# Performance work log

Hardware: AMD Instinct MI355X
Metric: run time of the kernel (lower is better)

Reference implementation:

```python
import jax, jax.numpy as jnp
import numpy as np

D_MODEL = 512; D_STATE = 128; D_CONV = 4; EXPAND = 2; HEADDIM = 64; CHUNK = 64
D_INNER = EXPAND * D_MODEL            # 1024
NHEADS = D_INNER // HEADDIM           # 16
CONV_DIM = D_INNER + 2 * D_STATE      # 1280
D_IN_PROJ = 2 * D_INNER + 2 * D_STATE + NHEADS  # 2320
BATCH, SEQLEN = 2, 8192


def setup_inputs() -> dict:
    key = jax.random.key(0)
    ks = jax.random.split(key, 8)
    s = 0.02
    return {
        "x": jax.random.normal(ks[0], (BATCH, SEQLEN, D_MODEL), jnp.float32),
        "in_proj_w": jax.random.normal(ks[1], (D_IN_PROJ, D_MODEL), jnp.float32) * s,
        "conv_w": jax.random.normal(ks[2], (CONV_DIM, 1, D_CONV), jnp.float32) * s,
        "conv_b": jnp.zeros((CONV_DIM,), jnp.float32),
        "dt_bias": jax.random.normal(ks[3], (NHEADS,), jnp.float32) * s,
        "A_log": jnp.log(jnp.arange(1, NHEADS + 1, dtype=jnp.float32)),
        "D_skip": jnp.ones((NHEADS,), jnp.float32),
        "norm_w": jnp.ones((D_INNER,), jnp.float32),
        "ssm_out_w": jax.random.normal(ks[4], (D_MODEL, D_INNER), jnp.float32) * s,
        "fuse_w": jax.random.normal(ks[5], (D_MODEL, 2 * D_MODEL), jnp.float32) * s,
        "fuse_b": jnp.zeros((D_MODEL,), jnp.float32),
    }


def segsum(a):
    # a: (..., T) -> (..., T, T) with [i, j] = sum_{j < d <= i} a[d]; -inf above diag
    T = a.shape[-1]
    a = jnp.broadcast_to(a[..., :, None], a.shape + (T,))
    a = jnp.where(jnp.tril(jnp.ones((T, T), bool), -1), a, 0.0)
    a = jnp.cumsum(a, axis=-2)
    return jnp.where(jnp.tril(jnp.ones((T, T), bool), 0), a, -jnp.inf)


def ssd(x, A, B, C):
    # x: (b,l,h,p), A: (b,l,h), B/C: (b,l,n) (single group, broadcast over heads)
    b, l, h, p = x.shape
    c = l // CHUNK
    x = x.reshape(b, c, CHUNK, h, p)
    A = jnp.transpose(A.reshape(b, c, CHUNK, h), (0, 3, 1, 2))   # (b,h,c,s)
    B = B.reshape(b, c, CHUNK, -1)
    C = C.reshape(b, c, CHUNK, -1)
    A_cumsum = jnp.cumsum(A, axis=-1)                             # (b,h,c,s)
    L = jnp.exp(segsum(A))                                        # (b,h,c,s,s) intra-chunk decay
    Y_diag = jnp.einsum("bcln,bcsn,bhcls,bcshp->bclhp", C, B, L, x)
    decay_states = jnp.exp(A_cumsum[..., -1:] - A_cumsum)         # (b,h,c,s)
    states = jnp.einsum("bcln,bhcl,bclhp->bchpn", B, decay_states, x)
    init = jnp.zeros_like(states[:, :1])
    A_pad = jnp.pad(A_cumsum[..., -1], ((0, 0), (0, 0), (1, 0)))  # (b,h,c+1)
    decay_chunk = jnp.exp(segsum(A_pad))                          # (b,h,c+1,c+1)
    new_states = jnp.einsum("bhzc,bchpn->bzhpn", decay_chunk,
                            jnp.concatenate([init, states], axis=1))
    states = new_states[:, :-1]                                   # state entering each chunk
    state_decay_out = jnp.exp(A_cumsum)
    Y_off = jnp.einsum("bchpn,bcsn,bhcs->bcshp", states, C, state_decay_out)
    return (Y_diag + Y_off).reshape(b, l, h, p)


def mamba2_block(u, in_proj_w, conv_w, conv_b, dt_bias, A_log, D_skip, norm_w, ssm_out_w):
    b, l, _ = u.shape
    zxbcdt = u @ in_proj_w.T                                      # (b,l,2320)
    z = zxbcdt[..., :D_INNER]
    xBC = zxbcdt[..., D_INNER:D_INNER + CONV_DIM]
    dt = jax.nn.softplus(zxbcdt[..., -NHEADS:] + dt_bias)         # (b,l,h)
    # depthwise causal conv over time
    conv = jax.lax.conv_general_dilated(
        jnp.transpose(xBC, (0, 2, 1)), conv_w, (1,), [(D_CONV - 1, 0)],
        dimension_numbers=("NCH", "OIH", "NCH"), feature_group_count=CONV_DIM)
    xBC = jax.nn.silu(jnp.transpose(conv + conv_b[None, :, None], (0, 2, 1)))
    xh = xBC[..., :D_INNER].reshape(b, l, NHEADS, HEADDIM)
    Bm = xBC[..., D_INNER:D_INNER + D_STATE]
    Cm = xBC[..., -D_STATE:]
    A = -jnp.exp(A_log)                                           # (h,)
    y = ssd(xh * dt[..., None], A * dt, Bm, Cm)
    y = y + xh * D_skip[None, None, :, None]
    y = y.reshape(b, l, D_INNER)
    # gated RMSNorm
    y = y * jax.nn.silu(z)
    y = y * jax.lax.rsqrt(jnp.mean(y * y, axis=-1, keepdims=True) + 1e-5) * norm_w
    return y @ ssm_out_w.T


def reference(x, in_proj_w, conv_w, conv_b, dt_bias, A_log, D_skip, norm_w,
              ssm_out_w, fuse_w, fuse_b):
    args = (in_proj_w, conv_w, conv_b, dt_bias, A_log, D_skip, norm_w, ssm_out_w)
    y_fwd = mamba2_block(x, *args)
    y_rev = jnp.flip(mamba2_block(jnp.flip(x, 1), *args), 1)
    y_cat = jnp.concatenate([y_fwd, y_rev], axis=-1)
    return y_cat @ fuse_w.T + fuse_b
```

## Files before the change

kernel.cpp:

```cpp
#include <hip/hip_runtime.h>
#include <cstddef>

#define B_SZ     2
#define L_SEQ    8192
#define D_INNERC 1024
#define D_CAT    2048
#define NHEADSC  16
#define CHUNKC   64
#define NCHUNKC  128
#define CONV_DIMC 1280
#define D_PROJC  2320
#define M_ROWS   16384

typedef unsigned short bfu;

using bf16x8 = __attribute__((ext_vector_type(8))) short;
using f32x4  = __attribute__((ext_vector_type(4))) float;

__device__ __forceinline__ float silu_(float v) { return v / (1.f + expf(-v)); }

__device__ __forceinline__ float b2f(bfu u) {
  return __uint_as_float((unsigned)u << 16);
}
__device__ __forceinline__ bfu f2b(float f) {
  unsigned x = __float_as_uint(f);
  return (bfu)((x + 0x7fffu + ((x >> 16) & 1u)) >> 16);
}

__device__ __forceinline__ float4 ld4(const float* p) { return *(const float4*)p; }
__device__ __forceinline__ float4 ld4(const bfu* p) {
  ushort4 u = *(const ushort4*)p;
  float4 f;
  f.x = b2f(u.x); f.y = b2f(u.y); f.z = b2f(u.z); f.w = b2f(u.w);
  return f;
}
__device__ __forceinline__ void st4(float* p, float4 v) { *(float4*)p = v; }
__device__ __forceinline__ void st4(bfu* p, float4 v) {
  ushort4 u;
  u.x = f2b(v.x); u.y = f2b(v.y); u.z = f2b(v.z); u.w = f2b(v.w);
  *(ushort4*)p = u;
}

__device__ __forceinline__ void gl_lds16(const bfu* g, bfu* l) {
  __builtin_amdgcn_global_load_lds(
      (const __attribute__((address_space(1))) unsigned int*)g,
      (__attribute__((address_space(3))) unsigned int*)l, 16, 0, 0);
}

__device__ __forceinline__ int pos_of(int b, int c, int l, int dir) {
  int t = c * CHUNKC + l;
  return dir ? (b * L_SEQ + (L_SEQ - 1) - t) : (b * L_SEQ + t);
}

__global__ __launch_bounds__(256)
void mfma_nt(const bfu* __restrict__ A, int lda,
             const bfu* __restrict__ Bw, int ldb,
             void* __restrict__ Cv, int ldc,
             int N, int K, const float* __restrict__ bias, int mode)
{
  __shared__ bfu sh[16384];
  bfu* As = sh;
  bfu* Bs = sh + 8192;
  const int tid  = threadIdx.x;
  const int lane = tid & 63;
  const int wave = __builtin_amdgcn_readfirstlane(tid >> 6);
  const int wm = wave & 1, wn = wave >> 1;

  const int num_n = gridDim.x;
  const int flat  = blockIdx.y * num_n + blockIdx.x;
  const int xcd   = flat & 7;
  const int g     = flat >> 3;
  const int n0 = (g % num_n) * 128;
  const int m0 = ((g / num_n) * 8 + xcd) * 128;

  f32x4 acc[4][4];
#pragma unroll
  for (int i = 0; i < 4; ++i)
#pragma unroll
    for (int j = 0; j < 4; ++j)
      acc[i][j] = (f32x4){0.f, 0.f, 0.f, 0.f};

  const int ro   = lane >> 3;
  const int slot = lane & 7;

  for (int k0 = 0; k0 < K; k0 += 64) {
    __syncthreads();
#pragma unroll
    for (int si = 0; si < 4; ++si) {
      int r = wave * 32 + si * 8 + ro;
      int cg = slot ^ (r & 7);
      gl_lds16(A  + (size_t)(m0 + r) * lda + k0 + cg * 8, As + (wave * 32 + si * 8) * 64);
      gl_lds16(Bw + (size_t)(n0 + r) * ldb + k0 + cg * 8, Bs + (wave * 32 + si * 8) * 64);
    }
    __syncthreads();

#pragma unroll
    for (int ks = 0; ks < 2; ++ks) {
      bf16x8 af[4], bfr[4];
#pragma unroll
      for (int i = 0; i < 4; ++i) {
        int ra = wm * 64 + i * 16 + (lane & 15);
        int ca = (ks * 4 + (lane >> 4)) ^ (ra & 7);
        af[i] = *(const bf16x8*)(As + ra * 64 + ca * 8);
        int rb = wn * 64 + i * 16 + (lane & 15);
        int cb = (ks * 4 + (lane >> 4)) ^ (rb & 7);
        bfr[i] = *(const bf16x8*)(Bs + rb * 64 + cb * 8);
      }
#pragma unroll
      for (int i = 0; i < 4; ++i)
#pragma unroll
        for (int j = 0; j < 4; ++j)
          acc[i][j] = __builtin_amdgcn_mfma_f32_16x16x32_bf16(af[i], bfr[j], acc[i][j], 0, 0, 0);
    }
  }

  __syncthreads();
  if (mode == 0) {
#pragma unroll
    for (int i = 0; i < 4; ++i)
#pragma unroll
      for (int j = 0; j < 4; ++j)
#pragma unroll
        for (int r = 0; r < 4; ++r) {
          int ml = wm * 64 + i * 16 + (lane >> 4) * 4 + r;
          int nl = wn * 64 + j * 16 + (lane & 15);
          sh[ml * 128 + nl] = f2b(acc[i][j][r]);
        }
    __syncthreads();
    bfu* Cb = (bfu*)Cv;
#pragma unroll
    for (int rr = 0; rr < 8; ++rr) {
      int idx = rr * 256 + tid;
      int row = idx >> 4, co = (idx & 15) * 8;
      if (n0 + co < N) {
        *(ulonglong2*)(Cb + (size_t)(m0 + row) * ldc + n0 + co) =
            *(const ulonglong2*)(sh + row * 128 + co);
      }
    }
  } else {
    float* Cf = (float*)Cv;
    float* shf = (float*)sh;
#pragma unroll
    for (int p = 0; p < 2; ++p) {
      if (wm == p) {
#pragma unroll
        for (int i = 0; i < 4; ++i)
#pragma unroll
          for (int j = 0; j < 4; ++j)
#pragma unroll
            for (int r = 0; r < 4; ++r) {
              int ml = i * 16 + (lane >> 4) * 4 + r;
              int nl = wn * 64 + j * 16 + (lane & 15);
              shf[ml * 128 + nl] = acc[i][j][r];
            }
      }
      __syncthreads();
#pragma unroll
      for (int rr = 0; rr < 8; ++rr) {
        int idx = rr * 256 + tid;
        int row = idx >> 5, co = (idx & 31) * 4;
        int n = n0 + co;
        if (n < N) {
          float4 v = *(float4*)(shf + row * 128 + co);
          float* cp = Cf + (size_t)(m0 + p * 64 + row) * ldc + n;
          if (bias) {
            v.x += bias[n]; v.y += bias[n + 1]; v.z += bias[n + 2]; v.w += bias[n + 3];
          }
          *(float4*)cp = v;
        }
      }
      __syncthreads();
    }
  }
}

__global__ __launch_bounds__(512)
void mfma_nt_8p(const bfu* __restrict__ A, int lda,
                const bfu* __restrict__ Bw, int ldb,
                bfu* __restrict__ C, int ldc, int N, int K)
{
  __shared__ bfu sh[65536];
  bfu* As0 = sh;
  bfu* As1 = sh + 16384;
  bfu* Bs0 = sh + 32768;
  bfu* Bs1 = sh + 49152;

  const int tid  = threadIdx.x;
  const int lane = tid & 63;
  const int w    = __builtin_amdgcn_readfirstlane(tid >> 6);
  const int wm = w & 1, wn = w >> 1;
  const int q = lane >> 4, t = lane & 15;

  const int num_n = gridDim.x;
  const int flat  = blockIdx.y * num_n + blockIdx.x;
  const int xcd   = flat & 7;
  const int g     = flat >> 3;
  const int n0 = (g % num_n) * 256;
  const int m0 = ((g / num_n) * 8 + xcd) * 256;

  auto STG = [&](const bfu* __restrict__ X, int ldx, int x0, int kt, int h,
                 bfu* dst) {
#pragma unroll
    for (int ci = 0; ci < 2; ++ci) {
      int rb = h * 128 + ci * 64 + w * 8;
      int r  = rb + (lane >> 3);
      int cg = (lane & 7) ^ (r & 7);
      gl_lds16(X + (size_t)(x0 + r) * ldx + kt * 64 + cg * 8, dst + rb * 64);
    }
  };
  auto FR = [&](const bfu* tile, int R, int gg) -> bf16x8 {
    return *(const bf16x8*)(tile + R * 64 + ((gg ^ (R & 7)) * 8));
  };

  f32x4 acc[8][4];
#pragma unroll
  for (int i = 0; i < 8; ++i)
#pragma unroll
    for (int j = 0; j < 4; ++j)
      acc[i][j] = (f32x4){0.f, 0.f, 0.f, 0.f};

  STG(Bw, ldb, n0, 0, 0, Bs0); STG(Bw, ldb, n0, 0, 1, Bs0);
  STG(A,  lda, m0, 0, 0, As0); STG(A,  lda, m0, 0, 1, As0);
  STG(Bw, ldb, n0, 1, 0, Bs1); STG(Bw, ldb, n0, 1, 1, Bs1);
  asm volatile("s_waitcnt vmcnt(4)" ::: "memory");
  __builtin_amdgcn_s_barrier();

  const int nIter = K >> 7;
  bf16x8 bfr[4][2];
  for (int it = 0; it < nIter; ++it) {
    const int kt = it * 2;
    const bool last = (it == nIter - 1);

#pragma unroll
    for (int p = 0; p < 4; ++p) {
      bf16x8 af[2][2];
#pragma unroll
      for (int ii = 0; ii < 2; ++ii)
#pragma unroll
        for (int ks = 0; ks < 2; ++ks)
          af[ii][ks] = FR(As0, wm * 128 + (2 * p + ii) * 16 + t, ks * 4 + q);
      if (p == 0) {
#pragma unroll
        for (int j = 0; j < 4; ++j)
#pragma unroll
          for (int ks = 0; ks < 2; ++ks)
            bfr[j][ks] = FR(Bs0, wn * 64 + j * 16 + t, ks * 4 + q);
      }
      if (p == 0)          STG(A,  lda, m0, kt + 1, 0, As1);
      if (p == 1)          STG(A,  lda, m0, kt + 1, 1, As1);
      if (p == 2 && !last) STG(Bw, ldb, n0, kt + 2, 0, Bs0);
      if (p == 3 && !last) STG(Bw, ldb, n0, kt + 2, 1, Bs0);
      if (p == 3) {
        if (last) asm volatile("s_waitcnt vmcnt(0)" ::: "memory");
        else      asm volatile("s_waitcnt vmcnt(4)" ::: "memory");
      }
      __builtin_amdgcn_s_barrier();
      __builtin_amdgcn_s_setprio(1);
#pragma unroll
      for (int ks = 0; ks < 2; ++ks)
#pragma unroll
        for (int ii = 0; ii < 2; ++ii)
#pragma unroll
          for (int j = 0; j < 4; ++j)
            acc[2 * p + ii][j] = __builtin_amdgcn_mfma_f32_16x16x32_bf16(
                af[ii][ks], bfr[j][ks], acc[2 * p + ii][j], 0, 0, 0);
      __builtin_amdgcn_s_setprio(0);
      __builtin_amdgcn_s_barrier();
    }

#pragma unroll
    for (int p = 0; p < 4; ++p) {
      bf16x8 af[2][2];
#pragma unroll
      for (int ii = 0; ii < 2; ++ii)
#pragma unroll
        for (int ks = 0; ks < 2; ++ks)
          af[ii][ks] = FR(As1, wm * 128 + (2 * p + ii) * 16 + t, ks * 4 + q);
      if (p == 0) {
#pragma unroll
        for (int j = 0; j < 4; ++j)
#pragma unroll
          for (int ks = 0; ks < 2; ++ks)
            bfr[j][ks] = FR(Bs1, wn * 64 + j * 16 + t, ks * 4 + q);
      }
      if (p == 0 && !last) STG(A,  lda, m0, kt + 2, 0, As0);
      if (p == 1 && !last) STG(A,  lda, m0, kt + 2, 1, As0);
      if (p == 2 && !last) STG(Bw, ldb, n0, kt + 3, 0, Bs1);
      if (p == 3 && !last) STG(Bw, ldb, n0, kt + 3, 1, Bs1);
      if (p == 3 && !last) asm volatile("s_waitcnt vmcnt(4)" ::: "memory");
      __builtin_amdgcn_s_barrier();
      __builtin_amdgcn_s_setprio(1);
#pragma unroll
      for (int ks = 0; ks < 2; ++ks)
#pragma unroll
        for (int ii = 0; ii < 2; ++ii)
#pragma unroll
          for (int j = 0; j < 4; ++j)
            acc[2 * p + ii][j] = __builtin_amdgcn_mfma_f32_16x16x32_bf16(
                af[ii][ks], bfr[j][ks], acc[2 * p + ii][j], 0, 0, 0);
      __builtin_amdgcn_s_setprio(0);
      __builtin_amdgcn_s_barrier();
    }
  }

#pragma unroll
  for (int i = 0; i < 8; ++i)
#pragma unroll
    for (int j = 0; j < 4; ++j)
#pragma unroll
      for (int r = 0; r < 4; ++r) {
        int ml = wm * 128 + i * 16 + q * 4 + r;
        int nl = wn * 64 + j * 16 + t;
        sh[ml * 256 + nl] = f2b(acc[i][j][r]);
      }
  __syncthreads();
#pragma unroll
  for (int rr = 0; rr < 16; ++rr) {
    int idx = rr * 512 + tid;
    int row = idx >> 5, co = (idx & 31) * 8;
    if (n0 + co < N) {
      *(ulonglong2*)(C + (size_t)(m0 + row) * ldc + n0 + co) =
          *(const ulonglong2*)(sh + row * 256 + co);
    }
  }
}

__global__ __launch_bounds__(256)
void cvt_x_k(const float* __restrict__ in, bfu* __restrict__ out)
{
  int q = blockIdx.x * 256 + threadIdx.x;
  st4(out + (size_t)q * 4, ld4(in + (size_t)q * 4));
}

__global__ __launch_bounds__(256)
void cvt_w_k(const float* __restrict__ in, bfu* __restrict__ out)
{
  int q = blockIdx.x * 256 + threadIdx.x;
  int row = q >> 7, c4 = (q & 127) << 2;
  float4 v = {0.f, 0.f, 0.f, 0.f};
  if (row < D_PROJC) v = ld4(in + (size_t)row * 512 + c4);
  st4(out + (size_t)row * 512 + c4, v);
}

__global__ __launch_bounds__(256)
void transpose_k(const float* __restrict__ in, bfu* __restrict__ out)
{
  int idx = blockIdx.x * 256 + threadIdx.x;
  int j = idx >> 9, k = idx & 511;
  out[idx] = f2b(in[k * 1024 + j]);
}

__global__ __launch_bounds__(256)
void cvt_fuse_k(const float* __restrict__ in, bfu* __restrict__ out)
{
  int q = blockIdx.x * 256 + threadIdx.x;
  int m = q >> 7, kg = (q & 127) << 2;
  int o = m >> 1, dir = m & 1;
  float4 v = ld4(in + (size_t)o * 1024 + dir * 512 + kg);
  st4(out + (size_t)m * 512 + kg, v);
}

__global__ __launch_bounds__(256)
void conv_k(const bfu* __restrict__ zx, const float* __restrict__ conv_w,
            const float* __restrict__ conv_b, bfu* __restrict__ xBC, int dir)
{
  int ch = blockIdx.x * 256 + threadIdx.x;
  int m0 = blockIdx.y * 8;
  int b  = m0 >> 13, tb = m0 & (L_SEQ - 1);
  float w0 = conv_w[ch * 4 + 0], w1 = conv_w[ch * 4 + 1];
  float w2 = conv_w[ch * 4 + 2], w3 = conv_w[ch * 4 + 3];
  float cb = conv_b[ch];
  const bfu* src = zx + 1024 + ch;
  const int shift = dir ? 0 : 3;

  float v[11];
#pragma unroll
  for (int i = 0; i < 11; ++i) {
    int tt = tb + i - shift;
    v[i] = (tt >= 0 && tt < L_SEQ)
         ? b2f(src[(size_t)(b * L_SEQ + tt) * D_PROJC]) : 0.f;
  }
#pragma unroll
  for (int j = 0; j < 8; ++j) {
    float acc = cb;
    if (dir == 0) {
      acc += w0 * v[j] + w1 * v[j + 1] + w2 * v[j + 2] + w3 * v[j + 3];
    } else {
      acc += w0 * v[j + 3] + w1 * v[j + 2] + w2 * v[j + 1] + w3 * v[j];
    }
    xBC[(size_t)(m0 + j) * CONV_DIMC + ch] = f2b(silu_(acc));
  }
}

__global__ __launch_bounds__(256)
void states_mfma_k(const bfu* __restrict__ zx, const bfu* __restrict__ xBC,
                   const float* __restrict__ dt_bias, const float* __restrict__ A_log,
                   float* __restrict__ acum_g, float* __restrict__ dt_g,
                   bfu* __restrict__ states, int dir)
{
  __shared__ bfu BT[128 * 72];
  __shared__ bfu xsT[64 * 72];
  __shared__ float scaleS[8 * 64];

  int bid = blockIdx.x;
  int hb = bid >> 8;
  int c = bid & 127, b = (bid >> 7) & 1;
  int tid = threadIdx.x, lane = tid & 63;
  int w = tid >> 6, q = lane >> 4, t = lane & 15;

#pragma unroll
  for (int rr = 0; rr < 2; ++rr) {
    int i = w + rr * 4;
    int h = hb * 8 + i;
    int l = lane;
    int pos = pos_of(b, c, l, dir);
    float dtr = b2f(zx[(size_t)pos * D_PROJC + 2304 + h]) + dt_bias[h];
    float dt = (dtr > 20.f) ? dtr : log1pf(expf(dtr));
    float a = -expf(A_log[h]) * dt;
#pragma unroll
    for (int off = 1; off < 64; off <<= 1) {
      float v = __shfl_up(a, off);
      if (l >= off) a += v;
    }
    float alast = __shfl(a, 63);
    int gi = ((b * NCHUNKC + c) * NHEADSC + h) * 64 + l;
    acum_g[gi] = a; dt_g[gi] = dt;
    scaleS[i * 64 + l] = dt * expf(alast - a);
  }

#pragma unroll
  for (int r = 0; r < 8; ++r) {
    int qq = tid + r * 256;
    int l = qq & 63, ng = qq >> 6;
    ushort4 v = *(const ushort4*)(xBC + (size_t)pos_of(b, c, l, dir) * CONV_DIMC + 1024 + ng * 4);
    BT[(ng * 4 + 0) * 72 + l] = v.x; BT[(ng * 4 + 1) * 72 + l] = v.y;
    BT[(ng * 4 + 2) * 72 + l] = v.z; BT[(ng * 4 + 3) * 72 + l] = v.w;
  }

  ushort4 xr[4];
  auto PREFX = [&](int i) {
    int h = hb * 8 + i;
#pragma unroll
    for (int r = 0; r < 4; ++r) {
      int qq = tid + r * 256;
      int l = qq & 63, pg = qq >> 6;
      xr[r] = *(const ushort4*)(xBC + (size_t)pos_of(b, c, l, dir) * CONV_DIMC + h * 64 + pg * 4);
    }
  };
  PREFX(0);
  __syncthreads();

  for (int i = 0; i < 8; ++i) {
    int h = hb * 8 + i;
#pragma unroll
    for (int r = 0; r < 4; ++r) {
      int qq = tid + r * 256;
      int l = qq & 63, pg = qq >> 6;
      float s = scaleS[i * 64 + l];
      ushort4 v = xr[r];
      xsT[(pg * 4 + 0) * 72 + l] = f2b(b2f(v.x) * s);
      xsT[(pg * 4 + 1) * 72 + l] = f2b(b2f(v.y) * s);
      xsT[(pg * 4 + 2) * 72 + l] = f2b(b2f(v.z) * s);
      xsT[(pg * 4 + 3) * 72 + l] = f2b(b2f(v.w) * s);
    }
    if (i < 7) PREFX(i + 1);
    __syncthreads();

    bf16x8 axs[2];
#pragma unroll
    for (int ks = 0; ks < 2; ++ks)
      axs[ks] = *(const bf16x8*)(xsT + (w * 16 + t) * 72 + ks * 32 + q * 8);

    f32x4 acc[8];
#pragma unroll
    for (int j = 0; j < 8; ++j) acc[j] = (f32x4){0.f, 0.f, 0.f, 0.f};
#pragma unroll
    for (int ks = 0; ks < 2; ++ks)
#pragma unroll
      for (int j = 0; j < 8; ++j) {
        bf16x8 bB = *(const bf16x8*)(BT + (j * 16 + t) * 72 + ks * 32 + q * 8);
        acc[j] = __builtin_amdgcn_mfma_f32_16x16x32_bf16(axs[ks], bB, acc[j], 0, 0, 0);
      }

    size_t base = ((size_t)(b * NCHUNKC + c) * NHEADSC + h) * 8192;
#pragma unroll
    for (int j = 0; j < 8; ++j)
#pragma unroll
      for (int r = 0; r < 4; ++r) {
        int p = w * 16 + q * 4 + r, n = j * 16 + t;
        states[base + p * 128 + n] = f2b(acc[j][r]);
      }
    __syncthreads();
  }
}

__global__ __launch_bounds__(256)
void scan_k(bfu* __restrict__ states, const float* __restrict__ acum_g)
{
  int bid = blockIdx.x;
  int eb = bid & 15, h = (bid >> 4) & 15, b = bid >> 8;
  int e = eb * 512 + threadIdx.x * 2;
  bfu* p0 = states + ((size_t)(b * NCHUNKC) * NHEADSC + h) * 8192 + e;
  const float* ac = acum_g + ((b * NCHUNKC) * NHEADSC + h) * 64 + 63;
  const size_t cstride = (size_t)NHEADSC * 8192;
  const int astride = NHEADSC * 64;

  float pre0 = 0.f, pre1 = 0.f;
  uint raw = *(const uint*)p0;
  float dcur = expf(ac[0]);
  for (int c = 0; c < NCHUNKC; ++c) {
    uint raw_next = 0; float dnext = 0.f;
    if (c < NCHUNKC - 1) {
      raw_next = *(const uint*)(p0 + (c + 1) * cstride);
      dnext = expf(ac[(c + 1) * astride]);
    }
    float v0 = b2f((bfu)(raw & 0xffff));
    float v1 = b2f((bfu)(raw >> 16));
    uint packed = (uint)f2b(pre0) | ((uint)f2b(pre1) << 16);
    *(uint*)(p0 + c * cstride) = packed;
    pre0 = v0 + dcur * pre0;
    pre1 = v1 + dcur * pre1;
    raw = raw_next; dcur = dnext;
  }
}

__global__ __launch_bounds__(256)
void y_mfma_k(const bfu* __restrict__ xBC, const bfu* __restrict__ states,
              const float* __restrict__ acum_g, const float* __restrict__ dt_g,
              const float* __restrict__ D_skip, bfu* __restrict__ ycat, int dir)
{
  __shared__ bfu smem[30976];
  bfu* Cs  = smem;
  bfu* Bsc = smem + 8704;
  bfu* Ps  = smem + 17408;
  bfu* xhT = smem + 26112;
  float* acumH = (float*)(smem + 30720);
  float* dtH   = acumH + 64;

  int bid = blockIdx.x;
  int hb = bid >> 8;
  int c = bid & 127, b = (bid >> 7) & 1;
  int tid = threadIdx.x, lane = tid & 63;
  int w = tid >> 6, q = lane >> 4, t = lane & 15;

#pragma unroll
  for (int r = 0; r < 8; ++r) {
    int qq = tid + r * 256;
    int row = qq >> 5, grp = qq & 31;
    const bfu* src = xBC + (size_t)pos_of(b, c, row, dir) * CONV_DIMC;
    *(ushort4*)(Cs  + row * 136 + grp * 4) = *(const ushort4*)(src + 1152 + grp * 4);
    *(ushort4*)(Bsc + row * 136 + grp * 4) = *(const ushort4*)(src + 1024 + grp * 4);
  }
  __syncthreads();

  bf16x8 af[4];
#pragma unroll
  for (int ks = 0; ks < 4; ++ks)
    af[ks] = *(const bf16x8*)(Cs + (w * 16 + t) * 136 + ks * 32 + q * 8);

  f32x4 sacc[4];
#pragma unroll
  for (int j = 0; j < 4; ++j) sacc[j] = (f32x4){0.f, 0.f, 0.f, 0.f};
#pragma unroll
  for (int ks = 0; ks < 4; ++ks)
#pragma unroll
    for (int j = 0; j < 4; ++j) {
      bf16x8 bf = *(const bf16x8*)(Bsc + (j * 16 + t) * 136 + ks * 32 + q * 8);
      sacc[j] = __builtin_amdgcn_mfma_f32_16x16x32_bf16(af[ks], bf, sacc[j], 0, 0, 0);
    }

  for (int i = 0; i < 8; ++i) {
    int h = hb * 8 + i;
    __syncthreads();
    size_t pbase = ((size_t)(b * NCHUNKC + c) * NHEADSC + h) * 8192;
#pragma unroll
    for (int r = 0; r < 8; ++r) {
      int qq = tid + r * 256;
      int row = qq >> 5, grp = qq & 31;
      *(ushort4*)(Ps + row * 136 + grp * 4) =
          *(const ushort4*)(states + pbase + row * 128 + grp * 4);
    }
#pragma unroll
    for (int r = 0; r < 4; ++r) {
      int qq = tid + r * 256;
      int l = qq & 63, pg = qq >> 6;
      ushort4 v = *(const ushort4*)(xBC + (size_t)pos_of(b, c, l, dir) * CONV_DIMC + h * 64 + pg * 4);
      xhT[(pg * 4 + 0) * 72 + l] = v.x; xhT[(pg * 4 + 1) * 72 + l] = v.y;
      xhT[(pg * 4 + 2) * 72 + l] = v.z; xhT[(pg * 4 + 3) * 72 + l] = v.w;
    }
    if (tid < 64) {
      int gi = ((b * NCHUNKC + c) * NHEADSC + h) * 64 + tid;
      acumH[tid] = acum_g[gi]; dtH[tid] = dt_g[gi];
    }
    __syncthreads();

    f32x4 yacc[4];
#pragma unroll
    for (int j = 0; j < 4; ++j) yacc[j] = (f32x4){0.f, 0.f, 0.f, 0.f};
#pragma unroll
    for (int ks = 0; ks < 4; ++ks)
#pragma unroll
      for (int j = 0; j < 4; ++j) {
        bf16x8 bP = *(const bf16x8*)(Ps + (j * 16 + t) * 136 + ks * 32 + q * 8);
        yacc[j] = __builtin_amdgcn_mfma_f32_16x16x32_bf16(af[ks], bP, yacc[j], 0, 0, 0);
      }

    float Dh = D_skip[h];
    bfu* sc = Bsc;
#pragma unroll
    for (int j = 0; j < 4; ++j)
#pragma unroll
      for (int r = 0; r < 4; ++r) {
        int l = w * 16 + q * 4 + r, s = j * 16 + t;
        float v = 0.f;
        if (s <= l) v = sacc[j][r] * expf(acumH[l] - acumH[s]) * dtH[s];
        if (s == l) v += Dh;
        sc[l * 72 + s] = f2b(v);
      }

    f32x4 acc2[4];
    float dec[4];
#pragma unroll
    for (int r = 0; r < 4; ++r) dec[r] = expf(acumH[w * 16 + q * 4 + r]);
#pragma unroll
    for (int j = 0; j < 4; ++j)
#pragma unroll
      for (int r = 0; r < 4; ++r) acc2[j][r] = yacc[j][r] * dec[r];

#pragma unroll
    for (int ks = 0; ks < 2; ++ks) {
      bf16x8 asc = *(const bf16x8*)(sc + (w * 16 + t) * 72 + ks * 32 + q * 8);
#pragma unroll
      for (int j = 0; j < 4; ++j) {
        bf16x8 bx = *(const bf16x8*)(xhT + (j * 16 + t) * 72 + ks * 32 + q * 8);
        acc2[j] = __builtin_amdgcn_mfma_f32_16x16x32_bf16(asc, bx, acc2[j], 0, 0, 0);
      }
    }

#pragma unroll
    for (int j = 0; j < 4; ++j)
#pragma unroll
      for (int r = 0; r < 4; ++r) {
        int l = w * 16 + q * 4 + r, p = j * 16 + t;
        ycat[(size_t)pos_of(b, c, l, dir) * D_CAT + dir * 1024 + h * 64 + p] =
            f2b(acc2[j][r]);
      }
  }
}

__global__ __launch_bounds__(256)
void norm_k(bfu* __restrict__ ycat, const bfu* __restrict__ zx,
            const float* __restrict__ norm_w, int dir)
{
  int m = blockIdx.x, tid = threadIdx.x;
  bfu* yp = ycat + (size_t)m * D_CAT + dir * 1024 + tid * 4;
  float4 y = ld4(yp);
  float4 z = ld4(zx + (size_t)m * D_PROJC + tid * 4);
  float4 g;
  g.x = y.x * silu_(z.x); g.y = y.y * silu_(z.y);
  g.z = y.z * silu_(z.z); g.w = y.w * silu_(z.w);
  float ss = g.x * g.x + g.y * g.y + g.z * g.z + g.w * g.w;
#pragma unroll
  for (int off = 32; off >= 1; off >>= 1) ss += __shfl_xor(ss, off);
  __shared__ float red[4];
  int wid = tid >> 6;
  if ((tid & 63) == 0) red[wid] = ss;
  __syncthreads();
  float tot = red[0] + red[1] + red[2] + red[3];
  float scale = rsqrtf(tot * (1.f / 1024.f) + 1e-5f);
  float4 w = *(const float4*)(norm_w + tid * 4);
  g.x *= scale * w.x; g.y *= scale * w.y; g.z *= scale * w.z; g.w *= scale * w.w;
  st4(yp, g);
}

extern "C" void kernel_launch(void* const* d_in, const int* in_sizes, int n_in,
                              void* d_out, int out_size, void* d_ws, size_t ws_size,
                              hipStream_t stream)
{
  const float* x         = (const float*)d_in[0];
  const float* in_proj_w = (const float*)d_in[1];
  const float* conv_w    = (const float*)d_in[2];
  const float* conv_b    = (const float*)d_in[3];
  const float* dt_bias   = (const float*)d_in[4];
  const float* A_log     = (const float*)d_in[5];
  const float* D_skip    = (const float*)d_in[6];
  const float* norm_w    = (const float*)d_in[7];
  const float* ssm_out_w = (const float*)d_in[8];
  const float* fuse_w    = (const float*)d_in[9];
  const float* fuse_b    = (const float*)d_in[10];
  float* out = (float*)d_out;

  bfu* zx     = (bfu*)d_ws;
  bfu* xBC    = zx     + (size_t)M_ROWS * D_PROJC;
  bfu* states = xBC    + (size_t)M_ROWS * CONV_DIMC;
  bfu* ycat   = states + (size_t)33554432;
  float* acum = (float*)(ycat + (size_t)M_ROWS * D_CAT);
  float* dtg  = acum + 262144;
  bfu* ssmTb  = (bfu*)(dtg + 262144);
  bfu* fuseA  = ssmTb + 524288;
  bfu* wcmb   = fuseA + 524288;
  bfu* xb = states;
  bfu* wb = states + 8388608;

  cvt_x_k<<<8192, 256, 0, stream>>>(x, xb);
  cvt_w_k<<<1280, 256, 0, stream>>>(in_proj_w, wb);
  transpose_k<<<2048, 256, 0, stream>>>(ssm_out_w, ssmTb);
  cvt_fuse_k<<<512, 256, 0, stream>>>(fuse_w, fuseA);

  mfma_nt<<<dim3(8, 8), 256, 0, stream>>>(
      fuseA, 512, ssmTb, 512, wcmb, 1024, 1024, 512, nullptr, 0);

  mfma_nt_8p<<<dim3(10, 64), 512, 0, stream>>>(
      xb, 512, wb, 512, zx, D_PROJC, D_PROJC, 512);

  for (int dir = 0; dir < 2; ++dir) {
    conv_k<<<dim3(5, 2048), 256, 0, stream>>>(zx, conv_w, conv_b, xBC, dir);
    states_mfma_k<<<512, 256, 0, stream>>>(zx, xBC, dt_bias, A_log, acum, dtg, states, dir);
    scan_k<<<512, 256, 0, stream>>>(states, acum);
    y_mfma_k<<<512, 256, 0, stream>>>(xBC, states, acum, dtg, D_skip, ycat, dir);
    norm_k<<<M_ROWS, 256, 0, stream>>>(ycat, zx, norm_w, dir);
  }

  mfma_nt<<<dim3(4, 128), 256, 0, stream>>>(
      ycat, D_CAT, wcmb, D_CAT, out, 512, 512, D_CAT, fuse_b, 1);
}
```

Before: 532.8 us.

## Batch forward and reverse directions into single kernel launches with duplicated buffers

Merges the two direction iterations of the conv, states, scan, y and norm kernels into single launches with twice the grid. Each direction gets its own xBC, states, acum and dt buffers when the workspace is large enough. This removes half the launches and doubles parallelism per launch, which matters most for the serial scan kernel, whose 512 blocks leave the GPU underfilled. The cost is more workspace memory, with a fallback to the old sequential scheme when the workspace is too small.

```diff
diff --git a/kernel.cpp b/kernel.cpp
--- a/kernel.cpp
+++ b/kernel.cpp
@@ -362,10 +362,14 @@
 
 __global__ __launch_bounds__(256)
 void conv_k(const bfu* __restrict__ zx, const float* __restrict__ conv_w,
-            const float* __restrict__ conv_b, bfu* __restrict__ xBC, int dir)
-{
+            const float* __restrict__ conv_b, bfu* __restrict__ xBC,
+            size_t xbc_str, int dir_lo)
+{
+  int di  = blockIdx.y >> 11;
+  int dir = dir_lo + di;
+  bfu* xBCd = xBC + (size_t)di * xbc_str;
   int ch = blockIdx.x * 256 + threadIdx.x;
-  int m0 = blockIdx.y * 8;
+  int m0 = (blockIdx.y & 2047) * 8;
   int b  = m0 >> 13, tb = m0 & (L_SEQ - 1);
   float w0 = conv_w[ch * 4 + 0], w1 = conv_w[ch * 4 + 1];
   float w2 = conv_w[ch * 4 + 2], w3 = conv_w[ch * 4 + 3];
@@ -388,21 +392,30 @@
     } else {
       acc += w0 * v[j + 3] + w1 * v[j + 2] + w2 * v[j + 1] + w3 * v[j];
     }
-    xBC[(size_t)(m0 + j) * CONV_DIMC + ch] = f2b(silu_(acc));
+    xBCd[(size_t)(m0 + j) * CONV_DIMC + ch] = f2b(silu_(acc));
   }
 }
 
 __global__ __launch_bounds__(256)
 void states_mfma_k(const bfu* __restrict__ zx, const bfu* __restrict__ xBC,
+                   size_t xbc_str,
                    const float* __restrict__ dt_bias, const float* __restrict__ A_log,
                    float* __restrict__ acum_g, float* __restrict__ dt_g,
-                   bfu* __restrict__ states, int dir)
+                   size_t ac_str,
+                   bfu* __restrict__ states, size_t st_str, int dir_lo)
 {
   __shared__ bfu BT[128 * 72];
   __shared__ bfu xsT[64 * 72];
   __shared__ float scaleS[8 * 64];
 
-  int bid = blockIdx.x;
+  int di  = blockIdx.x >> 9;
+  int dir = dir_lo + di;
+  const bfu* xBCd = xBC + (size_t)di * xbc_str;
+  float* acumd = acum_g + (size_t)di * ac_str;
+  float* dtgd  = dt_g   + (size_t)di * ac_str;
+  bfu* statesd = states + (size_t)di * st_str;
+
+  int bid = blockIdx.x & 511;
   int hb = bid >> 8;
   int c = bid & 127, b = (bid >> 7) & 1;
   int tid = threadIdx.x, lane = tid & 63;
@@ -424,7 +437,7 @@
     }
     float alast = __shfl(a, 63);
     int gi = ((b * NCHUNKC + c) * NHEADSC + h) * 64 + l;
-    acum_g[gi] = a; dt_g[gi] = dt;
+    acumd[gi] = a; dtgd[gi] = dt;
     scaleS[i * 64 + l] = dt * expf(alast - a);
   }
 
@@ -432,7 +445,7 @@
   for (int r = 0; r < 8; ++r) {
     int qq = tid + r * 256;
     int l = qq & 63, ng = qq >> 6;
-    ushort4 v = *(const ushort4*)(xBC + (size_t)pos_of(b, c, l, dir) * CONV_DIMC + 1024 + ng * 4);
+    ushort4 v = *(const ushort4*)(xBCd + (size_t)pos_of(b, c, l, dir) * CONV_DIMC + 1024 + ng * 4);
     BT[(ng * 4 + 0) * 72 + l] = v.x; BT[(ng * 4 + 1) * 72 + l] = v.y;
     BT[(ng * 4 + 2) * 72 + l] = v.z; BT[(ng * 4 + 3) * 72 + l] = v.w;
   }
@@ -444,7 +457,7 @@
     for (int r = 0; r < 4; ++r) {
       int qq = tid + r * 256;
       int l = qq & 63, pg = qq >> 6;
-      xr[r] = *(const ushort4*)(xBC + (size_t)pos_of(b, c, l, dir) * CONV_DIMC + h * 64 + pg * 4);
+      xr[r] = *(const ushort4*)(xBCd + (size_t)pos_of(b, c, l, dir) * CONV_DIMC + h * 64 + pg * 4);
     }
   };
   PREFX(0);
@@ -488,20 +501,25 @@
 #pragma unroll
       for (int r = 0; r < 4; ++r) {
         int p = w * 16 + q * 4 + r, n = j * 16 + t;
-        states[base + p * 128 + n] = f2b(acc[j][r]);
+        statesd[base + p * 128 + n] = f2b(acc[j][r]);
       }
     __syncthreads();
   }
 }
 
 __global__ __launch_bounds__(256)
-void scan_k(bfu* __restrict__ states, const float* __restrict__ acum_g)
-{
-  int bid = blockIdx.x;
+void scan_k(bfu* __restrict__ states, size_t st_str,
+            const float* __restrict__ acum_g, size_t ac_str)
+{
+  int di  = blockIdx.x >> 9;
+  int bid = blockIdx.x & 511;
+  bfu* statesd = states + (size_t)di * st_str;
+  const float* acumd = acum_g + (size_t)di * ac_str;
+
   int eb = bid & 15, h = (bid >> 4) & 15, b = bid >> 8;
   int e = eb * 512 + threadIdx.x * 2;
-  bfu* p0 = states + ((size_t)(b * NCHUNKC) * NHEADSC + h) * 8192 + e;
-  const float* ac = acum_g + ((b * NCHUNKC) * NHEADSC + h) * 64 + 63;
+  bfu* p0 = statesd + ((size_t)(b * NCHUNKC) * NHEADSC + h) * 8192 + e;
+  const float* ac = acumd + ((b * NCHUNKC) * NHEADSC + h) * 64 + 63;
   const size_t cstride = (size_t)NHEADSC * 8192;
   const int astride = NHEADSC * 64;
 
@@ -525,9 +543,11 @@
 }
 
 __global__ __launch_bounds__(256)
-void y_mfma_k(const bfu* __restrict__ xBC, const bfu* __restrict__ states,
+void y_mfma_k(const bfu* __restrict__ xBC, size_t xbc_str,
+              const bfu* __restrict__ states, size_t st_str,
               const float* __restrict__ acum_g, const float* __restrict__ dt_g,
-              const float* __restrict__ D_skip, bfu* __restrict__ ycat, int dir)
+              size_t ac_str,
+              const float* __restrict__ D_skip, bfu* __restrict__ ycat, int dir_lo)
 {
   __shared__ bfu smem[30976];
   bfu* Cs  = smem;
@@ -537,7 +557,14 @@
   float* acumH = (float*)(smem + 30720);
   float* dtH   = acumH + 64;
 
-  int bid = blockIdx.x;
+  int di  = blockIdx.x >> 9;
+  int dir = dir_lo + di;
+  const bfu* xBCd = xBC + (size_t)di * xbc_str;
+  const bfu* statesd = states + (size_t)di * st_str;
+  const float* acumd = acum_g + (size_t)di * ac_str;
+  const float* dtgd  = dt_g   + (size_t)di * ac_str;
+
+  int bid = blockIdx.x & 511;
   int hb = bid >> 8;
   int c = bid & 127, b = (bid >> 7) & 1;
   int tid = threadIdx.x, lane = tid & 63;
@@ -547,7 +574,7 @@
   for (int r = 0; r < 8; ++r) {
     int qq = tid + r * 256;
     int row = qq >> 5, grp = qq & 31;
-    const bfu* src = xBC + (size_t)pos_of(b, c, row, dir) * CONV_DIMC;
+    const bfu* src = xBCd + (size_t)pos_of(b, c, row, dir) * CONV_DIMC;
     *(ushort4*)(Cs  + row * 136 + grp * 4) = *(const ushort4*)(src + 1152 + grp * 4);
     *(ushort4*)(Bsc + row * 136 + grp * 4) = *(const ushort4*)(src + 1024 + grp * 4);
   }
@@ -578,19 +605,19 @@
       int qq = tid + r * 256;
       int row = qq >> 5, grp = qq & 31;
       *(ushort4*)(Ps + row * 136 + grp * 4) =
-          *(const ushort4*)(states + pbase + row * 128 + grp * 4);
+          *(const ushort4*)(statesd + pbase + row * 128 + grp * 4);
     }
 #pragma unroll
     for (int r = 0; r < 4; ++r) {
       int qq = tid + r * 256;
       int l = qq & 63, pg = qq >> 6;
-      ushort4 v = *(const ushort4*)(xBC + (size_t)pos_of(b, c, l, dir) * CONV_DIMC + h * 64 + pg * 4);
+      ushort4 v = *(const ushort4*)(xBCd + (size_t)pos_of(b, c, l, dir) * CONV_DIMC + h * 64 + pg * 4);
       xhT[(pg * 4 + 0) * 72 + l] = v.x; xhT[(pg * 4 + 1) * 72 + l] = v.y;
       xhT[(pg * 4 + 2) * 72 + l] = v.z; xhT[(pg * 4 + 3) * 72 + l] = v.w;
     }
     if (tid < 64) {
       int gi = ((b * NCHUNKC + c) * NHEADSC + h) * 64 + tid;
-      acumH[tid] = acum_g[gi]; dtH[tid] = dt_g[gi];
+      acumH[tid] = acumd[gi]; dtH[tid] = dtgd[gi];
     }
     __syncthreads();
 
@@ -650,9 +677,11 @@
 
 __global__ __launch_bounds__(256)
 void norm_k(bfu* __restrict__ ycat, const bfu* __restrict__ zx,
-            const float* __restrict__ norm_w, int dir)
-{
-  int m = blockIdx.x, tid = threadIdx.x;
+            const float* __restrict__ norm_w, int dir_lo)
+{
+  int di  = blockIdx.x >> 14;
+  int dir = dir_lo + di;
+  int m = blockIdx.x & 16383, tid = threadIdx.x;
   bfu* yp = ycat + (size_t)m * D_CAT + dir * 1024 + tid * 4;
   float4 y = ld4(yp);
   float4 z = ld4(zx + (size_t)m * D_PROJC + tid * 4);
@@ -690,18 +719,32 @@
   const float* fuse_b    = (const float*)d_in[10];
   float* out = (float*)d_out;
 
+  const size_t ZX_E  = (size_t)M_ROWS * D_PROJC;
+  const size_t XBC_E = (size_t)M_ROWS * CONV_DIMC;
+  const size_t ST_E  = 33554432;
+  const size_t YC_E  = (size_t)M_ROWS * D_CAT;
+  const size_t AC_E  = 262144;
+
+  size_t need2 = (ZX_E + 2 * XBC_E + 2 * ST_E + YC_E + 2 * 524288 + 1048576) * 2
+               + 4 * AC_E * 4;
+  const int nd = (ws_size >= need2) ? 2 : 1;
+
   bfu* zx     = (bfu*)d_ws;
-  bfu* xBC    = zx     + (size_t)M_ROWS * D_PROJC;
-  bfu* states = xBC    + (size_t)M_ROWS * CONV_DIMC;
-  bfu* ycat   = states + (size_t)33554432;
-  float* acum = (float*)(ycat + (size_t)M_ROWS * D_CAT);
-  float* dtg  = acum + 262144;
-  bfu* ssmTb  = (bfu*)(dtg + 262144);
+  bfu* xBC    = zx + ZX_E;
+  bfu* states = xBC + (size_t)nd * XBC_E;
+  bfu* ycat   = states + (size_t)nd * ST_E;
+  float* acum = (float*)(ycat + YC_E);
+  float* dtg  = acum + (size_t)nd * AC_E;
+  bfu* ssmTb  = (bfu*)(dtg + (size_t)nd * AC_E);
   bfu* fuseA  = ssmTb + 524288;
   bfu* wcmb   = fuseA + 524288;
   bfu* xb = states;
   bfu* wb = states + 8388608;
 
+  const size_t xbc_str = (nd == 2) ? XBC_E : 0;
+  const size_t st_str  = (nd == 2) ? ST_E  : 0;
+  const size_t ac_str  = (nd == 2) ? AC_E  : 0;
+
   cvt_x_k<<<8192, 256, 0, stream>>>(x, xb);
   cvt_w_k<<<1280, 256, 0, stream>>>(in_proj_w, wb);
   transpose_k<<<2048, 256, 0, stream>>>(ssm_out_w, ssmTb);
@@ -713,12 +756,15 @@
   mfma_nt_8p<<<dim3(10, 64), 512, 0, stream>>>(
       xb, 512, wb, 512, zx, D_PROJC, D_PROJC, 512);
 
-  for (int dir = 0; dir < 2; ++dir) {
-    conv_k<<<dim3(5, 2048), 256, 0, stream>>>(zx, conv_w, conv_b, xBC, dir);
-    states_mfma_k<<<512, 256, 0, stream>>>(zx, xBC, dt_bias, A_log, acum, dtg, states, dir);
-    scan_k<<<512, 256, 0, stream>>>(states, acum);
-    y_mfma_k<<<512, 256, 0, stream>>>(xBC, states, acum, dtg, D_skip, ycat, dir);
-    norm_k<<<M_ROWS, 256, 0, stream>>>(ycat, zx, norm_w, dir);
+  for (int dl = 0; dl < 2; dl += nd) {
+    conv_k<<<dim3(5, 2048 * nd), 256, 0, stream>>>(
+        zx, conv_w, conv_b, xBC, xbc_str, dl);
+    states_mfma_k<<<512 * nd, 256, 0, stream>>>(
+        zx, xBC, xbc_str, dt_bias, A_log, acum, dtg, ac_str, states, st_str, dl);
+    scan_k<<<512 * nd, 256, 0, stream>>>(states, st_str, acum, ac_str);
+    y_mfma_k<<<512 * nd, 256, 0, stream>>>(
+        xBC, xbc_str, states, st_str, acum, dtg, ac_str, D_skip, ycat, dl);
+    norm_k<<<16384 * nd, 256, 0, stream>>>(ycat, zx, norm_w, dl);
   }
 
   mfma_nt<<<dim3(4, 128), 256, 0, stream>>>(
```

New measurement: 521.1 us (median of 2 runs). -2.2%, faster.
